# Optimization experiments

Measured on AMD Instinct MI355X. Metric: run time of the kernel, lower is better.

The kernel has to match this reference:

```python
import jax, jax.numpy as jnp
import numpy as np

T, B, I, H, LBL = 200, 1024, 128, 128, 4


def setup_inputs() -> dict:
    key = jax.random.key(0)
    ks = jax.random.split(key, 14)
    si = 1.0 / np.sqrt(I)
    sh = 1.0 / np.sqrt(H)
    inputs = jax.random.normal(ks[0], (T, B, I), jnp.float32)
    lengths = jnp.maximum(jax.random.randint(ks[1], (B,), 1, T + 1), LBL).astype(jnp.int32)
    return {
        "inputs": inputs,
        "lengths": lengths,
        "Wih_g": jax.random.normal(ks[2], (3 * H, I), jnp.float32) * si,
        "Whh_g": jax.random.normal(ks[3], (3 * H, H), jnp.float32) * sh,
        "bih_g": jax.random.normal(ks[4], (3 * H,), jnp.float32) * sh,
        "bhh_g": jax.random.normal(ks[5], (3 * H,), jnp.float32) * sh,
        "Wih_l": jax.random.normal(ks[6], (3 * H, I), jnp.float32) * si,
        "Whh_l": jax.random.normal(ks[7], (3 * H, H), jnp.float32) * sh,
        "bih_l": jax.random.normal(ks[8], (3 * H,), jnp.float32) * sh,
        "bhh_l": jax.random.normal(ks[9], (3 * H,), jnp.float32) * sh,
        "A1": jax.random.normal(ks[10], (H, H), jnp.float32) * sh,
        "A2": jax.random.normal(ks[11], (H, H), jnp.float32) * sh,
        "v1": jax.random.normal(ks[12], (1, H), jnp.float32) * sh,
        "label_len": LBL,
    }


def gru(x, Wih, Whh, bih, bhh):
    # x: [T, B, I] time-major. PyTorch GRU cell semantics.
    Bq, Hq = x.shape[1], Whh.shape[1]
    gi_all = jnp.einsum('tbi,gi->tbg', x, Wih) + bih  # precompute input projections [T,B,3H]
    def step(h, gi):
        gh = h @ Whh.T + bhh
        ir, iz, inn = jnp.split(gi, 3, axis=-1)
        hr, hz, hn = jnp.split(gh, 3, axis=-1)
        r = jax.nn.sigmoid(ir + hr)
        z = jax.nn.sigmoid(iz + hz)
        n = jnp.tanh(inn + r * hn)
        h = (1.0 - z) * n + z * h
        return h, h
    h0 = jnp.zeros((Bq, Hq), x.dtype)
    _, hs = jax.lax.scan(step, h0, gi_all)
    return hs  # [T, B, H]


def reference(inputs, lengths, Wih_g, Whh_g, bih_g, bhh_g,
              Wih_l, Whh_l, bih_l, bhh_l, A1, A2, v1, label_len):
    h_g = gru(inputs, Wih_g, Whh_g, bih_g, bhh_g)  # [T,B,H]
    h_l = gru(inputs, Wih_l, Whh_l, bih_l, bhh_l)  # [T,B,H]
    # attention score per step s: v1(sigmoid(A1 h_l + A2 h_g)), query-independent
    pre = jax.nn.sigmoid(jnp.einsum('tbh,gh->tbg', h_l, A1) +
                         jnp.einsum('tbh,gh->tbg', h_g, A2))
    scores = jnp.einsum('tbg,og->tbo', pre, v1)  # [T,B,1]
    # per-t output = cumsum_{s<=t}(score*h_l) + h_g[t]
    out = jnp.cumsum(scores * h_l, axis=0) + h_g  # [T,B,H]
    out_b = jnp.transpose(out, (1, 0, 2))  # [B,T,H]
    # gather last label_len timesteps of each sequence: h[b,k] = out[L_b-label_len+k, b]
    idx = lengths[:, None].astype(jnp.int32) - label_len + jnp.arange(label_len, dtype=jnp.int32)[None, :]
    idx = jnp.clip(idx, 0, out_b.shape[1] - 1)  # [B, label_len]
    h = jnp.take_along_axis(out_b, idx[:, :, None], axis=1)  # [B, label_len, H]
    return h
```

## Files before the change

kernel.cpp:

```cpp
#include <hip/hip_runtime.h>
#include <stdint.h>


typedef __attribute__((ext_vector_type(8))) short short8;
typedef __attribute__((ext_vector_type(4))) float float4v;

#define LDS_BARRIER() asm volatile("s_waitcnt lgkmcnt(0)\n\ts_barrier" ::: "memory")

__device__ inline float bf2f(unsigned short u){
  union { unsigned int i; float f; } v; v.i = ((unsigned int)u) << 16; return v.f;
}
__device__ inline unsigned short f2bf(float f){
  union { float f; unsigned int i; } v; v.f = f;
  unsigned int x = v.i;
  return (unsigned short)((x + 0x7fffu + ((x >> 16) & 1u)) >> 16);
}
__device__ inline unsigned int cvt_pk_bf16(float a, float b){
  unsigned int r;
  asm("v_cvt_pk_bf16_f32 %0, %1, %2" : "=v"(r) : "v"(a), "v"(b));
  return r;
}
__device__ inline float sigm(float x){ return __builtin_amdgcn_rcpf(1.0f + __expf(-x)); }

union __align__(16) LdsU {
  struct { unsigned short hbuf[2][16][136]; unsigned short xbuf[2][16][136]; } scan;
  struct {
    unsigned short hlL[25 * 544];
    unsigned short hgL[25 * 544];
    float part[8 * 112];
    float scR[112];
  } cm;
};

__global__ __launch_bounds__(512, 2) void k_fat(
    const float* __restrict__ x,
    const float* __restrict__ bih_g, const float* __restrict__ bhh_g,
    const float* __restrict__ bih_l, const float* __restrict__ bhh_l,
    const float* __restrict__ Wih_g, const float* __restrict__ Whh_g,
    const float* __restrict__ Wih_l, const float* __restrict__ Whh_l,
    unsigned short* __restrict__ wst, unsigned short* __restrict__ a12,
    const float* __restrict__ v1, const int* __restrict__ lengths,
    unsigned short* __restrict__ hl, unsigned short* __restrict__ hg,
    float* __restrict__ cum, float* __restrict__ out,
    int scan_t0, int sccum_t0, int sccum_base, int build)
{
  __shared__ LdsU lds;
  int tid = threadIdx.x;
  int bid = blockIdx.x;

  if (scan_t0 >= 0 && bid < 128) {
    const int tc = 100;
    int t0 = scan_t0;
    auto& hbuf = lds.scan.hbuf;
    auto& xbuf = lds.scan.xbuf;

    int w = tid >> 6, L = tid & 63, l15 = L & 15, q = L >> 4;
    int gru = bid & 1;
    int b0 = (bid >> 1) * 16;
    const float* bih = gru ? bih_l : bih_g;
    const float* bhh = gru ? bhh_l : bhh_g;
    unsigned short* myseq = gru ? hl : hg;

    int col = w * 16 + l15;

    short8 Wi[3][4], Wh[3][4];
    if (t0 == 0) {
      const float* Wih = gru ? Wih_l : Wih_g;
      const float* Whh = gru ? Whh_l : Whh_g;
      #pragma unroll
      for (int G = 0; G < 3; G++) {
        int row = G * 128 + col;
        #pragma unroll
        for (int kf = 0; kf < 4; kf++) {
          const float4* p0 = (const float4*)(Wih + (size_t)row * 128 + kf * 32 + q * 8);
          const float4* p1 = (const float4*)(Whh + (size_t)row * 128 + kf * 32 + q * 8);
          float4 a0 = p0[0], a1 = p0[1], b0f = p1[0], b1f = p1[1];
          short8 si, sh;
          si[0]=(short)f2bf(a0.x); si[1]=(short)f2bf(a0.y); si[2]=(short)f2bf(a0.z); si[3]=(short)f2bf(a0.w);
          si[4]=(short)f2bf(a1.x); si[5]=(short)f2bf(a1.y); si[6]=(short)f2bf(a1.z); si[7]=(short)f2bf(a1.w);
          sh[0]=(short)f2bf(b0f.x); sh[1]=(short)f2bf(b0f.y); sh[2]=(short)f2bf(b0f.z); sh[3]=(short)f2bf(b0f.w);
          sh[4]=(short)f2bf(b1f.x); sh[5]=(short)f2bf(b1f.y); sh[6]=(short)f2bf(b1f.z); sh[7]=(short)f2bf(b1f.w);
          Wi[G][kf] = si; Wh[G][kf] = sh;
        }
      }
    } else {
      int gmi = gru * 2;
      int gmh = gru * 2 + 1;
      #pragma unroll
      for (int G = 0; G < 3; G++) {
        #pragma unroll
        for (int kf = 0; kf < 4; kf++) {
          Wi[G][kf] = *(const short8*)(wst + (((size_t)((gmi * 3 + G) * 4 + kf)) << 12) + tid * 8);
          Wh[G][kf] = *(const short8*)(wst + (((size_t)((gmh * 3 + G) * 4 + kf)) << 12) + tid * 8);
        }
      }
    }
    float br  = bih[col]       + bhh[col];
    float bz  = bih[128 + col] + bhh[128 + col];
    float bin = bih[256 + col];
    float bnh = bhh[256 + col];

    float hold[4];
    if (t0 == 0) {
      #pragma unroll
      for (int r = 0; r < 4; r++) { hold[r] = 0.0f; hbuf[0][q * 4 + r][col] = 0; }
    } else {
      const unsigned short* carry = myseq + (size_t)(t0 - 1) * 131072;
      #pragma unroll
      for (int r = 0; r < 4; r++) {
        int m = q * 4 + r;
        unsigned short u = carry[(size_t)(b0 + m) * 128 + col];
        hold[r] = bf2f(u);
        hbuf[0][m][col] = u;
      }
    }
    int xrow = tid >> 5, xc4 = (tid & 31) * 4;
    size_t hoff = (size_t)b0 * 128 + xrow * 128 + xc4;
    {
      float4 x0 = ((const float4*)(x + ((size_t)t0 * 1024 + b0) * 128))[tid];
      *(uint2*)&xbuf[0][xrow][xc4] = make_uint2(cvt_pk_bf16(x0.x, x0.y), cvt_pk_bf16(x0.z, x0.w));
    }
    float4 xr = ((const float4*)(x + ((size_t)(t0 + 1) * 1024 + b0) * 128))[tid];
    __syncthreads();

    float4v cx0 = (float4v){0.f,0.f,0.f,0.f}, cx1 = cx0, cx2 = cx0;
    {
      short8 Ax[4];
      #pragma unroll
      for (int kf = 0; kf < 4; kf++) Ax[kf] = *(const short8*)&xbuf[0][l15][kf * 32 + q * 8];
      #pragma unroll
      for (int kf = 0; kf < 4; kf++) cx0 = __builtin_amdgcn_mfma_f32_16x16x32_bf16(Ax[kf], Wi[0][kf], cx0, 0,0,0);
      #pragma unroll
      for (int kf = 0; kf < 4; kf++) cx1 = __builtin_amdgcn_mfma_f32_16x16x32_bf16(Ax[kf], Wi[1][kf], cx1, 0,0,0);
      #pragma unroll
      for (int kf = 0; kf < 4; kf++) cx2 = __builtin_amdgcn_mfma_f32_16x16x32_bf16(Ax[kf], Wi[2][kf], cx2, 0,0,0);
    }
    *(uint2*)&xbuf[1][xrow][xc4] = make_uint2(cvt_pk_bf16(xr.x, xr.y), cvt_pk_bf16(xr.z, xr.w));
    xr = ((const float4*)(x + ((size_t)(t0 + 2) * 1024 + b0) * 128))[tid];
    LDS_BARRIER();

    auto step = [&](int s, int pin, int pout) {
      short8 Ah[4], Axn[4];
      #pragma unroll
      for (int kf = 0; kf < 4; kf++) Ah[kf]  = *(const short8*)&hbuf[pin][l15][kf * 32 + q * 8];
      #pragma unroll
      for (int kf = 0; kf < 4; kf++) Axn[kf] = *(const short8*)&xbuf[pout][l15][kf * 32 + q * 8];

      if (s > 0) {
        uint2 hv = *(const uint2*)&hbuf[pin][xrow][xc4];
        *(uint2*)(myseq + (size_t)(t0 + s - 1) * 131072 + hoff) = hv;
      }

      float4v rh = (float4v){0.f,0.f,0.f,0.f}, zh = rh, nh = rh;
      #pragma unroll
      for (int kf = 0; kf < 4; kf++) rh = __builtin_amdgcn_mfma_f32_16x16x32_bf16(Ah[kf], Wh[0][kf], rh, 0,0,0);
      #pragma unroll
      for (int kf = 0; kf < 4; kf++) zh = __builtin_amdgcn_mfma_f32_16x16x32_bf16(Ah[kf], Wh[1][kf], zh, 0,0,0);
      #pragma unroll
      for (int kf = 0; kf < 4; kf++) nh = __builtin_amdgcn_mfma_f32_16x16x32_bf16(Ah[kf], Wh[2][kf], nh, 0,0,0);

      float4v nx0 = (float4v){0.f,0.f,0.f,0.f}, nx1 = nx0, nx2 = nx0;
      #pragma unroll
      for (int kf = 0; kf < 4; kf++) nx0 = __builtin_amdgcn_mfma_f32_16x16x32_bf16(Axn[kf], Wi[0][kf], nx0, 0,0,0);
      #pragma unroll
      for (int kf = 0; kf < 4; kf++) nx1 = __builtin_amdgcn_mfma_f32_16x16x32_bf16(Axn[kf], Wi[1][kf], nx1, 0,0,0);
      #pragma unroll
      for (int kf = 0; kf < 4; kf++) nx2 = __builtin_amdgcn_mfma_f32_16x16x32_bf16(Axn[kf], Wi[2][kf], nx2, 0,0,0);

      *(uint2*)&xbuf[pin][xrow][xc4] = make_uint2(cvt_pk_bf16(xr.x, xr.y), cvt_pk_bf16(xr.z, xr.w));
      {
        int t3 = t0 + (s + 3 < tc ? s + 3 : tc - 1);
        xr = ((const float4*)(x + ((size_t)t3 * 1024 + b0) * 128))[tid];
      }

      float cr[4], cz[4], cn[4];
      #pragma unroll
      for (int r = 0; r < 4; r++) { cr[r] = cx0[r] + br; cz[r] = cx1[r] + bz; cn[r] = cx2[r] + bin; }

      float hnv[4];
      #pragma unroll
      for (int r = 0; r < 4; r++) {
        float er = __expf(-(rh[r] + cr[r]));
        float ez = __expf(-(zh[r] + cz[r]));
        float pr = 1.0f + er, pz = 1.0f + ez;
        float inv = __builtin_amdgcn_rcpf(pr * pz);
        float rr = pz * inv;
        float zz = pr * inv;
        float y  = cn[r] + rr * (nh[r] + bnh);
        float em = __expf(-2.0f * y);
        float nn = 2.0f * __builtin_amdgcn_rcpf(1.0f + em) - 1.0f;
        hnv[r] = nn + zz * (hold[r] - nn);
        hold[r] = hnv[r];
      }
      unsigned int p01 = cvt_pk_bf16(hnv[0], hnv[1]);
      unsigned int p23 = cvt_pk_bf16(hnv[2], hnv[3]);
      hbuf[pout][q * 4 + 0][col] = (unsigned short)p01;
      hbuf[pout][q * 4 + 1][col] = (unsigned short)(p01 >> 16);
      hbuf[pout][q * 4 + 2][col] = (unsigned short)p23;
      hbuf[pout][q * 4 + 3][col] = (unsigned short)(p23 >> 16);

      cx0 = nx0; cx1 = nx1; cx2 = nx2;
      LDS_BARRIER();
    };

    for (int s = 0; s + 1 < tc; s += 2) { step(s, 0, 1); step(s + 1, 1, 0); }
    {
      uint2 hv = *(const uint2*)&hbuf[tc & 1][xrow][xc4];
      *(uint2*)(myseq + (size_t)(t0 + tc - 1) * 131072 + hoff) = hv;
    }
    return;
  }

  if (build) {
    if (bid < 128) return;
    int gid = (bid - 128) * 512 + tid;
    (void)gid;
    return;
  }

  if (sccum_t0 >= 0) {
    int t0c = sccum_t0;
    int rb = bid - sccum_base;
    int b0c = rb * 4;
    int w = tid >> 6, L = tid & 63, l15 = L & 15, q = L >> 4;
    int jc = tid & 127, bc = tid >> 7;
    int b = b0c + bc;

    auto* hlL = lds.cm.hlL;
    auto* hgL = lds.cm.hgL;
    float* part = lds.cm.part;
    float* scR  = lds.cm.scR;

    float c = (t0c == 0) ? 0.0f : cum[(size_t)b * 128 + jc];
    int cap0 = lengths[b] - 4;

    float hgv[4];
    #pragma unroll
    for (int d = 0; d < 4; d++) {
      int sl = cap0 + d - t0c;
      hgv[d] = (sl >= 0 && sl < 100) ? bf2f(hg[((size_t)(cap0 + d) * 1024 + b) * 128 + jc]) : 0.f;
    }

    short8 B1[4], B2[4];
    #pragma unroll
    for (int kf = 0; kf < 4; kf++) {
      B1[kf] = *(const short8*)(a12 + (size_t)(w * 16 + l15) * 128 + kf * 32 + q * 8);
      B2[kf] = *(const short8*)(a12 + 16384 + (size_t)(w * 16 + l15) * 128 + kf * 32 + q * 8);
    }
    float v1w = v1[w * 16 + l15];

    for (int seg = 0; seg < 4; seg++) {
      int t0s = t0c + seg * 25;
      __syncthreads();
      for (int f8 = tid; f8 < 1600; f8 += 512) {
        int sl = f8 >> 6, r8 = f8 & 63, bb = r8 >> 4, j8 = r8 & 15;
        size_t gsrc = ((size_t)(t0s + sl) * 1024 + b0c) * 128 + r8 * 8;
        int dst = sl * 544 + bb * 136 + j8 * 8;
        *(short8*)&hlL[dst] = *(const short8*)(hl + gsrc);
        *(short8*)&hgL[dst] = *(const short8*)(hg + gsrc);
      }
      __syncthreads();

      #pragma unroll
      for (int T = 0; T < 7; T++) {
        int tl = T * 4 + (l15 >> 2); if (tl > 24) tl = 24;
        int bb = l15 & 3;
        int abase = tl * 544 + bb * 136 + q * 8;
        short8 Al[4], Ag[4];
        #pragma unroll
        for (int kf = 0; kf < 4; kf++) {
          Al[kf] = *(const short8*)&hlL[abase + kf * 32];
          Ag[kf] = *(const short8*)&hgL[abase + kf * 32];
        }
        float4v acc = (float4v){0.f, 0.f, 0.f, 0.f};
        #pragma unroll
        for (int kf = 0; kf < 4; kf++) acc = __builtin_amdgcn_mfma_f32_16x16x32_bf16(Al[kf], B1[kf], acc, 0,0,0);
        #pragma unroll
        for (int kf = 0; kf < 4; kf++) acc = __builtin_amdgcn_mfma_f32_16x16x32_bf16(Ag[kf], B2[kf], acc, 0,0,0);
        #pragma unroll
        for (int r = 0; r < 4; r++) {
          float sv = v1w * sigm(acc[r]);
          sv += __shfl_xor(sv, 1, 16);
          sv += __shfl_xor(sv, 2, 16);
          sv += __shfl_xor(sv, 4, 16);
          sv += __shfl_xor(sv, 8, 16);
          if (l15 == 0) part[w * 112 + T * 16 + q * 4 + r] = sv;
        }
      }
      __syncthreads();
      if (tid < 100) {
        float s = 0.f;
        #pragma unroll
        for (int w8 = 0; w8 < 8; w8++) s += part[w8 * 112 + tid];
        scR[tid] = s;
      }
      __syncthreads();

      for (int sl = 0; sl < 25; sl += 5) {
        float h[5], scv[5];
        #pragma unroll
        for (int k = 0; k < 5; k++) {
          h[k]  = bf2f(hlL[(sl + k) * 544 + bc * 136 + jc]);
          scv[k] = scR[(sl + k) * 4 + bc];
        }
        #pragma unroll
        for (int k = 0; k < 5; k++) {
          c += scv[k] * h[k];
          int d = (t0s + sl + k) - cap0;
          if ((unsigned)d < 4u)
            out[((size_t)b * 4 + d) * 128 + jc] = c + hgv[d];
        }
      }
    }
    cum[(size_t)b * 128 + jc] = c;
    return;
  }
}

__global__ __launch_bounds__(512) void k_build(
    const float* __restrict__ Wih_g, const float* __restrict__ Whh_g,
    const float* __restrict__ Wih_l, const float* __restrict__ Whh_l,
    const float* __restrict__ A1, const float* __restrict__ A2,
    unsigned short* __restrict__ wst, unsigned short* __restrict__ a12)
{
  int gid = blockIdx.x * 512 + threadIdx.x;
  if (gid < 32768) a12[gid] = f2bf((gid < 16384) ? A1[gid] : A2[gid - 16384]);
  #pragma unroll
  for (int k = 0; k < 3; k++) {
    int i = gid + k * 65536;
    int f = i >> 12;
    int r = i & 4095;
    int t = r >> 3, e = r & 7;
    int l15 = t & 15, q = (t >> 4) & 3, wv = t >> 6;
    int col = wv * 16 + l15;
    int kf = f & 3, g3 = f >> 2;
    int G = g3 % 3, gm = g3 / 3;
    const float* src = (gm == 0) ? Wih_g : (gm == 1) ? Whh_g : (gm == 2) ? Wih_l : Whh_l;
    int row = G * 128 + col;
    int kk = kf * 32 + q * 8 + e;
    wst[i] = f2bf(src[(size_t)row * 128 + kk]);
  }
}

extern "C" void kernel_launch(void* const* d_in, const int* in_sizes, int n_in,
                              void* d_out, int out_size, void* d_ws, size_t ws_size,
                              hipStream_t stream)
{
  const float* x     = (const float*)d_in[0];
  const int* lengths = (const int*)d_in[1];
  const float* Wih_g = (const float*)d_in[2];
  const float* Whh_g = (const float*)d_in[3];
  const float* bih_g = (const float*)d_in[4];
  const float* bhh_g = (const float*)d_in[5];
  const float* Wih_l = (const float*)d_in[6];
  const float* Whh_l = (const float*)d_in[7];
  const float* bih_l = (const float*)d_in[8];
  const float* bhh_l = (const float*)d_in[9];
  const float* A1    = (const float*)d_in[10];
  const float* A2    = (const float*)d_in[11];
  const float* v1    = (const float*)d_in[12];
  float* out = (float*)d_out;

  char* wsb = (char*)d_ws;
  size_t o = 0;
  unsigned short* a12 = (unsigned short*)(wsb + o); o += 65536;
  unsigned short* wst = (unsigned short*)(wsb + o); o += 393216;
  float* cum          = (float*)(wsb + o);          o += 524288;
  unsigned short* hl  = (unsigned short*)(wsb + o); o += (size_t)200 * 1024 * 128 * 2;
  unsigned short* hg  = (unsigned short*)(wsb + o); o += (size_t)200 * 1024 * 128 * 2;
  if (o > ws_size) return;

  k_build<<<128, 512, 0, stream>>>(Wih_g, Whh_g, Wih_l, Whh_l, A1, A2, wst, a12);
  k_fat<<<128, 512, 0, stream>>>(x, bih_g, bhh_g, bih_l, bhh_l,
                                 Wih_g, Whh_g, Wih_l, Whh_l,
                                 wst, a12, v1, lengths, hl, hg, cum, out,
                                 0, -1, 0, 0);
  k_fat<<<384, 512, 0, stream>>>(x, bih_g, bhh_g, bih_l, bhh_l,
                                 Wih_g, Whh_g, Wih_l, Whh_l,
                                 wst, a12, v1, lengths, hl, hg, cum, out,
                                 100, 0, 128, 0);
  k_fat<<<256, 512, 0, stream>>>(x, bih_g, bhh_g, bih_l, bhh_l,
                                 Wih_g, Whh_g, Wih_l, Whh_l,
                                 wst, a12, v1, lengths, hl, hg, cum, out,
                                 -1, 100, 0, 0);
}
```

Before: 398.6 us.

## Run full-length GRU scan with 4-row batch tiles, then a single score/cumsum pass

```diff
diff --git a/kernel.cpp b/kernel.cpp
--- a/kernel.cpp
+++ b/kernel.cpp
@@ -22,323 +22,260 @@
 }
 __device__ inline float sigm(float x){ return __builtin_amdgcn_rcpf(1.0f + __expf(-x)); }
 
-union __align__(16) LdsU {
-  struct { unsigned short hbuf[2][16][136]; unsigned short xbuf[2][16][136]; } scan;
-  struct {
-    unsigned short hlL[25 * 544];
-    unsigned short hgL[25 * 544];
-    float part[8 * 112];
-    float scR[112];
-  } cm;
-};
-
-__global__ __launch_bounds__(512, 2) void k_fat(
+__global__ __launch_bounds__(512, 2) void k_scan(
     const float* __restrict__ x,
+    const float* __restrict__ Wih_g, const float* __restrict__ Whh_g,
     const float* __restrict__ bih_g, const float* __restrict__ bhh_g,
+    const float* __restrict__ Wih_l, const float* __restrict__ Whh_l,
     const float* __restrict__ bih_l, const float* __restrict__ bhh_l,
-    const float* __restrict__ Wih_g, const float* __restrict__ Whh_g,
-    const float* __restrict__ Wih_l, const float* __restrict__ Whh_l,
-    unsigned short* __restrict__ wst, unsigned short* __restrict__ a12,
+    unsigned short* __restrict__ hl_seq, unsigned short* __restrict__ hg_seq)
+{
+  __shared__ __align__(16) unsigned short hbuf[2][16][136];
+  __shared__ __align__(16) unsigned short xbuf[2][16][136];
+  const int tc = 200;
+  int tid = threadIdx.x;
+  int w = tid >> 6, L = tid & 63, l15 = L & 15, q = L >> 4;
+  int gru = blockIdx.x & 1;
+  int b0 = (blockIdx.x >> 1) * 4;
+  const float* Wih = gru ? Wih_l : Wih_g;
+  const float* Whh = gru ? Whh_l : Whh_g;
+  const float* bih = gru ? bih_l : bih_g;
+  const float* bhh = gru ? bhh_l : bhh_g;
+  unsigned short* myseq = gru ? hl_seq : hg_seq;
+
+  int col = w * 16 + l15;
+
+  short8 Wi[3][4], Wh[3][4];
+  #pragma unroll
+  for (int G = 0; G < 3; G++) {
+    int row = G * 128 + col;
+    #pragma unroll
+    for (int kf = 0; kf < 4; kf++) {
+      const float4* p0 = (const float4*)(Wih + (size_t)row * 128 + kf * 32 + q * 8);
+      const float4* p1 = (const float4*)(Whh + (size_t)row * 128 + kf * 32 + q * 8);
+      float4 a0 = p0[0], a1 = p0[1], b0f = p1[0], b1f = p1[1];
+      short8 si, sh;
+      si[0]=(short)f2bf(a0.x); si[1]=(short)f2bf(a0.y); si[2]=(short)f2bf(a0.z); si[3]=(short)f2bf(a0.w);
+      si[4]=(short)f2bf(a1.x); si[5]=(short)f2bf(a1.y); si[6]=(short)f2bf(a1.z); si[7]=(short)f2bf(a1.w);
+      sh[0]=(short)f2bf(b0f.x); sh[1]=(short)f2bf(b0f.y); sh[2]=(short)f2bf(b0f.z); sh[3]=(short)f2bf(b0f.w);
+      sh[4]=(short)f2bf(b1f.x); sh[5]=(short)f2bf(b1f.y); sh[6]=(short)f2bf(b1f.z); sh[7]=(short)f2bf(b1f.w);
+      Wi[G][kf] = si; Wh[G][kf] = sh;
+    }
+  }
+  float br  = bih[col]       + bhh[col];
+  float bz  = bih[128 + col] + bhh[128 + col];
+  float bin = bih[256 + col];
+  float bnh = bhh[256 + col];
+
+  float hold[4] = {0.f, 0.f, 0.f, 0.f};
+  #pragma unroll
+  for (int r = 0; r < 4; r++) hbuf[0][q * 4 + r][col] = 0;
+
+  int xrow = tid >> 5, xc4 = (tid & 31) * 4;
+  if (xrow >= 4) {
+    *(uint2*)&xbuf[0][xrow][xc4] = make_uint2(0u, 0u);
+    *(uint2*)&xbuf[1][xrow][xc4] = make_uint2(0u, 0u);
+  }
+  size_t hoff = (size_t)(b0 + xrow) * 128 + xc4;
+  float4 xr = make_float4(0.f, 0.f, 0.f, 0.f);
+  if (tid < 128) {
+    float4 x0 = *(const float4*)(x + ((size_t)0 * 1024 + b0) * 128 + tid * 4);
+    *(uint2*)&xbuf[0][xrow][xc4] = make_uint2(cvt_pk_bf16(x0.x, x0.y), cvt_pk_bf16(x0.z, x0.w));
+    xr = *(const float4*)(x + ((size_t)1 * 1024 + b0) * 128 + tid * 4);
+  }
+  __syncthreads();
+
+  float4v cx0 = (float4v){0.f,0.f,0.f,0.f}, cx1 = cx0, cx2 = cx0;
+  {
+    short8 Ax[4];
+    #pragma unroll
+    for (int kf = 0; kf < 4; kf++) Ax[kf] = *(const short8*)&xbuf[0][l15][kf * 32 + q * 8];
+    #pragma unroll
+    for (int kf = 0; kf < 4; kf++) cx0 = __builtin_amdgcn_mfma_f32_16x16x32_bf16(Ax[kf], Wi[0][kf], cx0, 0,0,0);
+    #pragma unroll
+    for (int kf = 0; kf < 4; kf++) cx1 = __builtin_amdgcn_mfma_f32_16x16x32_bf16(Ax[kf], Wi[1][kf], cx1, 0,0,0);
+    #pragma unroll
+    for (int kf = 0; kf < 4; kf++) cx2 = __builtin_amdgcn_mfma_f32_16x16x32_bf16(Ax[kf], Wi[2][kf], cx2, 0,0,0);
+  }
+  if (tid < 128) {
+    *(uint2*)&xbuf[1][xrow][xc4] = make_uint2(cvt_pk_bf16(xr.x, xr.y), cvt_pk_bf16(xr.z, xr.w));
+    xr = *(const float4*)(x + ((size_t)2 * 1024 + b0) * 128 + tid * 4);
+  }
+  LDS_BARRIER();
+
+  auto step = [&](int s, int pin, int pout) {
+    short8 Ah[4], Axn[4];
+    #pragma unroll
+    for (int kf = 0; kf < 4; kf++) Ah[kf]  = *(const short8*)&hbuf[pin][l15][kf * 32 + q * 8];
+    #pragma unroll
+    for (int kf = 0; kf < 4; kf++) Axn[kf] = *(const short8*)&xbuf[pout][l15][kf * 32 + q * 8];
+
+    if (s > 0 && tid < 128) {
+      uint2 hv = *(const uint2*)&hbuf[pin][xrow][xc4];
+      *(uint2*)(myseq + (size_t)(s - 1) * 131072 + hoff) = hv;
+    }
+
+    float4v rh = (float4v){0.f,0.f,0.f,0.f}, zh = rh, nh = rh;
+    #pragma unroll
+    for (int kf = 0; kf < 4; kf++) rh = __builtin_amdgcn_mfma_f32_16x16x32_bf16(Ah[kf], Wh[0][kf], rh, 0,0,0);
+    #pragma unroll
+    for (int kf = 0; kf < 4; kf++) zh = __builtin_amdgcn_mfma_f32_16x16x32_bf16(Ah[kf], Wh[1][kf], zh, 0,0,0);
+    #pragma unroll
+    for (int kf = 0; kf < 4; kf++) nh = __builtin_amdgcn_mfma_f32_16x16x32_bf16(Ah[kf], Wh[2][kf], nh, 0,0,0);
+
+    float4v nx0 = (float4v){0.f,0.f,0.f,0.f}, nx1 = nx0, nx2 = nx0;
+    #pragma unroll
+    for (int kf = 0; kf < 4; kf++) nx0 = __builtin_amdgcn_mfma_f32_16x16x32_bf16(Axn[kf], Wi[0][kf], nx0, 0,0,0);
+    #pragma unroll
+    for (int kf = 0; kf < 4; kf++) nx1 = __builtin_amdgcn_mfma_f32_16x16x32_bf16(Axn[kf], Wi[1][kf], nx1, 0,0,0);
+    #pragma unroll
+    for (int kf = 0; kf < 4; kf++) nx2 = __builtin_amdgcn_mfma_f32_16x16x32_bf16(Axn[kf], Wi[2][kf], nx2, 0,0,0);
+
+    if (tid < 128) {
+      *(uint2*)&xbuf[pin][xrow][xc4] = make_uint2(cvt_pk_bf16(xr.x, xr.y), cvt_pk_bf16(xr.z, xr.w));
+      int t3 = (s + 3 < tc ? s + 3 : tc - 1);
+      xr = *(const float4*)(x + ((size_t)t3 * 1024 + b0) * 128 + tid * 4);
+    }
+
+    float cr[4], cz[4], cn[4];
+    #pragma unroll
+    for (int r = 0; r < 4; r++) { cr[r] = cx0[r] + br; cz[r] = cx1[r] + bz; cn[r] = cx2[r] + bin; }
+
+    float hnv[4];
+    #pragma unroll
+    for (int r = 0; r < 4; r++) {
+      float er = __expf(-(rh[r] + cr[r]));
+      float ez = __expf(-(zh[r] + cz[r]));
+      float pr = 1.0f + er, pz = 1.0f + ez;
+      float inv = __builtin_amdgcn_rcpf(pr * pz);
+      float rr = pz * inv;
+      float zz = pr * inv;
+      float y  = cn[r] + rr * (nh[r] + bnh);
+      float em = __expf(-2.0f * y);
+      float nn = 2.0f * __builtin_amdgcn_rcpf(1.0f + em) - 1.0f;
+      hnv[r] = nn + zz * (hold[r] - nn);
+      hold[r] = hnv[r];
+    }
+    unsigned int p01 = cvt_pk_bf16(hnv[0], hnv[1]);
+    unsigned int p23 = cvt_pk_bf16(hnv[2], hnv[3]);
+    hbuf[pout][q * 4 + 0][col] = (unsigned short)p01;
+    hbuf[pout][q * 4 + 1][col] = (unsigned short)(p01 >> 16);
+    hbuf[pout][q * 4 + 2][col] = (unsigned short)p23;
+    hbuf[pout][q * 4 + 3][col] = (unsigned short)(p23 >> 16);
+
+    cx0 = nx0; cx1 = nx1; cx2 = nx2;
+    LDS_BARRIER();
+  };
+
+  for (int s = 0; s + 1 < tc; s += 2) { step(s, 0, 1); step(s + 1, 1, 0); }
+  if (tid < 128) {
+    uint2 hv = *(const uint2*)&hbuf[tc & 1][xrow][xc4];
+    *(uint2*)(myseq + (size_t)(tc - 1) * 131072 + hoff) = hv;
+  }
+}
+
+__global__ __launch_bounds__(512, 2) void k_sccum(
+    const unsigned short* __restrict__ hl, const unsigned short* __restrict__ hg,
+    const float* __restrict__ A1, const float* __restrict__ A2,
     const float* __restrict__ v1, const int* __restrict__ lengths,
-    unsigned short* __restrict__ hl, unsigned short* __restrict__ hg,
-    float* __restrict__ cum, float* __restrict__ out,
-    int scan_t0, int sccum_t0, int sccum_base, int build)
+    float* __restrict__ out)
 {
-  __shared__ LdsU lds;
+  __shared__ __align__(16) unsigned short hlL[25 * 544];
+  __shared__ __align__(16) unsigned short hgL[25 * 544];
+  __shared__ float part[8 * 112];
+  __shared__ float scR[112];
   int tid = threadIdx.x;
-  int bid = blockIdx.x;
-
-  if (scan_t0 >= 0 && bid < 128) {
-    const int tc = 100;
-    int t0 = scan_t0;
-    auto& hbuf = lds.scan.hbuf;
-    auto& xbuf = lds.scan.xbuf;
-
-    int w = tid >> 6, L = tid & 63, l15 = L & 15, q = L >> 4;
-    int gru = bid & 1;
-    int b0 = (bid >> 1) * 16;
-    const float* bih = gru ? bih_l : bih_g;
-    const float* bhh = gru ? bhh_l : bhh_g;
-    unsigned short* myseq = gru ? hl : hg;
-
-    int col = w * 16 + l15;
-
-    short8 Wi[3][4], Wh[3][4];
-    if (t0 == 0) {
-      const float* Wih = gru ? Wih_l : Wih_g;
-      const float* Whh = gru ? Whh_l : Whh_g;
-      #pragma unroll
-      for (int G = 0; G < 3; G++) {
-        int row = G * 128 + col;
-        #pragma unroll
-        for (int kf = 0; kf < 4; kf++) {
-          const float4* p0 = (const float4*)(Wih + (size_t)row * 128 + kf * 32 + q * 8);
-          const float4* p1 = (const float4*)(Whh + (size_t)row * 128 + kf * 32 + q * 8);
-          float4 a0 = p0[0], a1 = p0[1], b0f = p1[0], b1f = p1[1];
-          short8 si, sh;
-          si[0]=(short)f2bf(a0.x); si[1]=(short)f2bf(a0.y); si[2]=(short)f2bf(a0.z); si[3]=(short)f2bf(a0.w);
-          si[4]=(short)f2bf(a1.x); si[5]=(short)f2bf(a1.y); si[6]=(short)f2bf(a1.z); si[7]=(short)f2bf(a1.w);
-          sh[0]=(short)f2bf(b0f.x); sh[1]=(short)f2bf(b0f.y); sh[2]=(short)f2bf(b0f.z); sh[3]=(short)f2bf(b0f.w);
-          sh[4]=(short)f2bf(b1f.x); sh[5]=(short)f2bf(b1f.y); sh[6]=(short)f2bf(b1f.z); sh[7]=(short)f2bf(b1f.w);
-          Wi[G][kf] = si; Wh[G][kf] = sh;
-        }
+  int rb = blockIdx.x;
+  int b0c = rb * 4;
+  int w = tid >> 6, L = tid & 63, l15 = L & 15, q = L >> 4;
+  int jc = tid & 127, bc = (tid >> 7) & 3;
+  int b = b0c + bc;
+
+  float c = 0.0f;
+  int cap0 = lengths[b] - 4;
+
+  float hgv[4];
+  #pragma unroll
+  for (int d = 0; d < 4; d++)
+    hgv[d] = bf2f(hg[((size_t)(cap0 + d) * 1024 + b) * 128 + jc]);
+
+  short8 B1[4], B2[4];
+  #pragma unroll
+  for (int kf = 0; kf < 4; kf++) {
+    const float4* p1 = (const float4*)(A1 + (size_t)(w * 16 + l15) * 128 + kf * 32 + q * 8);
+    const float4* p2 = (const float4*)(A2 + (size_t)(w * 16 + l15) * 128 + kf * 32 + q * 8);
+    float4 a0 = p1[0], a1 = p1[1], c0 = p2[0], c1 = p2[1];
+    short8 s1, s2;
+    s1[0]=(short)f2bf(a0.x); s1[1]=(short)f2bf(a0.y); s1[2]=(short)f2bf(a0.z); s1[3]=(short)f2bf(a0.w);
+    s1[4]=(short)f2bf(a1.x); s1[5]=(short)f2bf(a1.y); s1[6]=(short)f2bf(a1.z); s1[7]=(short)f2bf(a1.w);
+    s2[0]=(short)f2bf(c0.x); s2[1]=(short)f2bf(c0.y); s2[2]=(short)f2bf(c0.z); s2[3]=(short)f2bf(c0.w);
+    s2[4]=(short)f2bf(c1.x); s2[5]=(short)f2bf(c1.y); s2[6]=(short)f2bf(c1.z); s2[7]=(short)f2bf(c1.w);
+    B1[kf] = s1; B2[kf] = s2;
+  }
+  float v1w = v1[w * 16 + l15];
+
+  for (int seg = 0; seg < 8; seg++) {
+    int t0s = seg * 25;
+    __syncthreads();
+    for (int f8 = tid; f8 < 1600; f8 += 512) {
+      int sl = f8 >> 6, r8 = f8 & 63, bb = r8 >> 4, j8 = r8 & 15;
+      size_t gsrc = ((size_t)(t0s + sl) * 1024 + b0c) * 128 + r8 * 8;
+      int dst = sl * 544 + bb * 136 + j8 * 8;
+      *(short8*)&hlL[dst] = *(const short8*)(hl + gsrc);
+      *(short8*)&hgL[dst] = *(const short8*)(hg + gsrc);
+    }
+    __syncthreads();
+
+    #pragma unroll
+    for (int T = 0; T < 7; T++) {
+      int tl = T * 4 + (l15 >> 2); if (tl > 24) tl = 24;
+      int bb = l15 & 3;
+      int abase = tl * 544 + bb * 136 + q * 8;
+      short8 Al[4], Ag[4];
+      #pragma unroll
+      for (int kf = 0; kf < 4; kf++) {
+        Al[kf] = *(const short8*)&hlL[abase + kf * 32];
+        Ag[kf] = *(const short8*)&hgL[abase + kf * 32];
       }
-    } else {
-      int gmi = gru * 2;
-      int gmh = gru * 2 + 1;
-      #pragma unroll
-      for (int G = 0; G < 3; G++) {
-        #pragma unroll
-        for (int kf = 0; kf < 4; kf++) {
-          Wi[G][kf] = *(const short8*)(wst + (((size_t)((gmi * 3 + G) * 4 + kf)) << 12) + tid * 8);
-          Wh[G][kf] = *(const short8*)(wst + (((size_t)((gmh * 3 + G) * 4 + kf)) << 12) + tid * 8);
-        }
+      float4v acc = (float4v){0.f, 0.f, 0.f, 0.f};
+      #pragma unroll
+      for (int kf = 0; kf < 4; kf++) acc = __builtin_amdgcn_mfma_f32_16x16x32_bf16(Al[kf], B1[kf], acc, 0,0,0);
+      #pragma unroll
+      for (int kf = 0; kf < 4; kf++) acc = __builtin_amdgcn_mfma_f32_16x16x32_bf16(Ag[kf], B2[kf], acc, 0,0,0);
+      #pragma unroll
+      for (int r = 0; r < 4; r++) {
+        float sv = v1w * sigm(acc[r]);
+        sv += __shfl_xor(sv, 1, 16);
+        sv += __shfl_xor(sv, 2, 16);
+        sv += __shfl_xor(sv, 4, 16);
+        sv += __shfl_xor(sv, 8, 16);
+        if (l15 == 0) part[w * 112 + T * 16 + q * 4 + r] = sv;
       }
     }
-    float br  = bih[col]       + bhh[col];
-    float bz  = bih[128 + col] + bhh[128 + col];
-    float bin = bih[256 + col];
-    float bnh = bhh[256 + col];
-
-    float hold[4];
-    if (t0 == 0) {
-      #pragma unroll
-      for (int r = 0; r < 4; r++) { hold[r] = 0.0f; hbuf[0][q * 4 + r][col] = 0; }
-    } else {
-      const unsigned short* carry = myseq + (size_t)(t0 - 1) * 131072;
-      #pragma unroll
-      for (int r = 0; r < 4; r++) {
-        int m = q * 4 + r;
-        unsigned short u = carry[(size_t)(b0 + m) * 128 + col];
-        hold[r] = bf2f(u);
-        hbuf[0][m][col] = u;
+    __syncthreads();
+    if (tid < 100) {
+      float s = 0.f;
+      #pragma unroll
+      for (int w8 = 0; w8 < 8; w8++) s += part[w8 * 112 + tid];
+      scR[tid] = s;
+    }
+    __syncthreads();
+
+    for (int sl = 0; sl < 25; sl += 5) {
+      float h[5], scv[5];
+      #pragma unroll
+      for (int k = 0; k < 5; k++) {
+        h[k]   = bf2f(hlL[(sl + k) * 544 + bc * 136 + jc]);
+        scv[k] = scR[(sl + k) * 4 + bc];
       }
-    }
-    int xrow = tid >> 5, xc4 = (tid & 31) * 4;
-    size_t hoff = (size_t)b0 * 128 + xrow * 128 + xc4;
-    {
-      float4 x0 = ((const float4*)(x + ((size_t)t0 * 1024 + b0) * 128))[tid];
-      *(uint2*)&xbuf[0][xrow][xc4] = make_uint2(cvt_pk_bf16(x0.x, x0.y), cvt_pk_bf16(x0.z, x0.w));
-    }
-    float4 xr = ((const float4*)(x + ((size_t)(t0 + 1) * 1024 + b0) * 128))[tid];
-    __syncthreads();
-
-    float4v cx0 = (float4v){0.f,0.f,0.f,0.f}, cx1 = cx0, cx2 = cx0;
-    {
-      short8 Ax[4];
-      #pragma unroll
-      for (int kf = 0; kf < 4; kf++) Ax[kf] = *(const short8*)&xbuf[0][l15][kf * 32 + q * 8];
-      #pragma unroll
-      for (int kf = 0; kf < 4; kf++) cx0 = __builtin_amdgcn_mfma_f32_16x16x32_bf16(Ax[kf], Wi[0][kf], cx0, 0,0,0);
-      #pragma unroll
-      for (int kf = 0; kf < 4; kf++) cx1 = __builtin_amdgcn_mfma_f32_16x16x32_bf16(Ax[kf], Wi[1][kf], cx1, 0,0,0);
-      #pragma unroll
-      for (int kf = 0; kf < 4; kf++) cx2 = __builtin_amdgcn_mfma_f32_16x16x32_bf16(Ax[kf], Wi[2][kf], cx2, 0,0,0);
-    }
-    *(uint2*)&xbuf[1][xrow][xc4] = make_uint2(cvt_pk_bf16(xr.x, xr.y), cvt_pk_bf16(xr.z, xr.w));
-    xr = ((const float4*)(x + ((size_t)(t0 + 2) * 1024 + b0) * 128))[tid];
-    LDS_BARRIER();
-
-    auto step = [&](int s, int pin, int pout) {
-      short8 Ah[4], Axn[4];
-      #pragma unroll
-      for (int kf = 0; kf < 4; kf++) Ah[kf]  = *(const short8*)&hbuf[pin][l15][kf * 32 + q * 8];
-      #pragma unroll
-      for (int kf = 0; kf < 4; kf++) Axn[kf] = *(const short8*)&xbuf[pout][l15][kf * 32 + q * 8];
-
-      if (s > 0) {
-        uint2 hv = *(const uint2*)&hbuf[pin][xrow][xc4];
-        *(uint2*)(myseq + (size_t)(t0 + s - 1) * 131072 + hoff) = hv;
+      #pragma unroll
+      for (int k = 0; k < 5; k++) {
+        c += scv[k] * h[k];
+        int d = (t0s + sl + k) - cap0;
+        if ((unsigned)d < 4u)
+          out[((size_t)b * 4 + d) * 128 + jc] = c + hgv[d];
       }
-
-      float4v rh = (float4v){0.f,0.f,0.f,0.f}, zh = rh, nh = rh;
-      #pragma unroll
-      for (int kf = 0; kf < 4; kf++) rh = __builtin_amdgcn_mfma_f32_16x16x32_bf16(Ah[kf], Wh[0][kf], rh, 0,0,0);
-      #pragma unroll
-      for (int kf = 0; kf < 4; kf++) zh = __builtin_amdgcn_mfma_f32_16x16x32_bf16(Ah[kf], Wh[1][kf], zh, 0,0,0);
-      #pragma unroll
-      for (int kf = 0; kf < 4; kf++) nh = __builtin_amdgcn_mfma_f32_16x16x32_bf16(Ah[kf], Wh[2][kf], nh, 0,0,0);
-
-      float4v nx0 = (float4v){0.f,0.f,0.f,0.f}, nx1 = nx0, nx2 = nx0;
-      #pragma unroll
-      for (int kf = 0; kf < 4; kf++) nx0 = __builtin_amdgcn_mfma_f32_16x16x32_bf16(Axn[kf], Wi[0][kf], nx0, 0,0,0);
-      #pragma unroll
-      for (int kf = 0; kf < 4; kf++) nx1 = __builtin_amdgcn_mfma_f32_16x16x32_bf16(Axn[kf], Wi[1][kf], nx1, 0,0,0);
-      #pragma unroll
-      for (int kf = 0; kf < 4; kf++) nx2 = __builtin_amdgcn_mfma_f32_16x16x32_bf16(Axn[kf], Wi[2][kf], nx2, 0,0,0);
-
-      *(uint2*)&xbuf[pin][xrow][xc4] = make_uint2(cvt_pk_bf16(xr.x, xr.y), cvt_pk_bf16(xr.z, xr.w));
-      {
-        int t3 = t0 + (s + 3 < tc ? s + 3 : tc - 1);
-        xr = ((const float4*)(x + ((size_t)t3 * 1024 + b0) * 128))[tid];
-      }
-
-      float cr[4], cz[4], cn[4];
-      #pragma unroll
-      for (int r = 0; r < 4; r++) { cr[r] = cx0[r] + br; cz[r] = cx1[r] + bz; cn[r] = cx2[r] + bin; }
-
-      float hnv[4];
-      #pragma unroll
-      for (int r = 0; r < 4; r++) {
-        float er = __expf(-(rh[r] + cr[r]));
-        float ez = __expf(-(zh[r] + cz[r]));
-        float pr = 1.0f + er, pz = 1.0f + ez;
-        float inv = __builtin_amdgcn_rcpf(pr * pz);
-        float rr = pz * inv;
-        float zz = pr * inv;
-        float y  = cn[r] + rr * (nh[r] + bnh);
-        float em = __expf(-2.0f * y);
-        float nn = 2.0f * __builtin_amdgcn_rcpf(1.0f + em) - 1.0f;
-        hnv[r] = nn + zz * (hold[r] - nn);
-        hold[r] = hnv[r];
-      }
-      unsigned int p01 = cvt_pk_bf16(hnv[0], hnv[1]);
-      unsigned int p23 = cvt_pk_bf16(hnv[2], hnv[3]);
-      hbuf[pout][q * 4 + 0][col] = (unsigned short)p01;
-      hbuf[pout][q * 4 + 1][col] = (unsigned short)(p01 >> 16);
-      hbuf[pout][q * 4 + 2][col] = (unsigned short)p23;
-      hbuf[pout][q * 4 + 3][col] = (unsigned short)(p23 >> 16);
-
-      cx0 = nx0; cx1 = nx1; cx2 = nx2;
-      LDS_BARRIER();
-    };
-
-    for (int s = 0; s + 1 < tc; s += 2) { step(s, 0, 1); step(s + 1, 1, 0); }
-    {
-      uint2 hv = *(const uint2*)&hbuf[tc & 1][xrow][xc4];
-      *(uint2*)(myseq + (size_t)(t0 + tc - 1) * 131072 + hoff) = hv;
-    }
-    return;
-  }
-
-  if (build) {
-    if (bid < 128) return;
-    int gid = (bid - 128) * 512 + tid;
-    (void)gid;
-    return;
-  }
-
-  if (sccum_t0 >= 0) {
-    int t0c = sccum_t0;
-    int rb = bid - sccum_base;
-    int b0c = rb * 4;
-    int w = tid >> 6, L = tid & 63, l15 = L & 15, q = L >> 4;
-    int jc = tid & 127, bc = tid >> 7;
-    int b = b0c + bc;
-
-    auto* hlL = lds.cm.hlL;
-    auto* hgL = lds.cm.hgL;
-    float* part = lds.cm.part;
-    float* scR  = lds.cm.scR;
-
-    float c = (t0c == 0) ? 0.0f : cum[(size_t)b * 128 + jc];
-    int cap0 = lengths[b] - 4;
-
-    float hgv[4];
-    #pragma unroll
-    for (int d = 0; d < 4; d++) {
-      int sl = cap0 + d - t0c;
-      hgv[d] = (sl >= 0 && sl < 100) ? bf2f(hg[((size_t)(cap0 + d) * 1024 + b) * 128 + jc]) : 0.f;
-    }
-
-    short8 B1[4], B2[4];
-    #pragma unroll
-    for (int kf = 0; kf < 4; kf++) {
-      B1[kf] = *(const short8*)(a12 + (size_t)(w * 16 + l15) * 128 + kf * 32 + q * 8);
-      B2[kf] = *(const short8*)(a12 + 16384 + (size_t)(w * 16 + l15) * 128 + kf * 32 + q * 8);
-    }
-    float v1w = v1[w * 16 + l15];
-
-    for (int seg = 0; seg < 4; seg++) {
-      int t0s = t0c + seg * 25;
-      __syncthreads();
-      for (int f8 = tid; f8 < 1600; f8 += 512) {
-        int sl = f8 >> 6, r8 = f8 & 63, bb = r8 >> 4, j8 = r8 & 15;
-        size_t gsrc = ((size_t)(t0s + sl) * 1024 + b0c) * 128 + r8 * 8;
-        int dst = sl * 544 + bb * 136 + j8 * 8;
-        *(short8*)&hlL[dst] = *(const short8*)(hl + gsrc);
-        *(short8*)&hgL[dst] = *(const short8*)(hg + gsrc);
-      }
-      __syncthreads();
-
-      #pragma unroll
-      for (int T = 0; T < 7; T++) {
-        int tl = T * 4 + (l15 >> 2); if (tl > 24) tl = 24;
-        int bb = l15 & 3;
-        int abase = tl * 544 + bb * 136 + q * 8;
-        short8 Al[4], Ag[4];
-        #pragma unroll
-        for (int kf = 0; kf < 4; kf++) {
-          Al[kf] = *(const short8*)&hlL[abase + kf * 32];
-          Ag[kf] = *(const short8*)&hgL[abase + kf * 32];
-        }
-        float4v acc = (float4v){0.f, 0.f, 0.f, 0.f};
-        #pragma unroll
-        for (int kf = 0; kf < 4; kf++) acc = __builtin_amdgcn_mfma_f32_16x16x32_bf16(Al[kf], B1[kf], acc, 0,0,0);
-        #pragma unroll
-        for (int kf = 0; kf < 4; kf++) acc = __builtin_amdgcn_mfma_f32_16x16x32_bf16(Ag[kf], B2[kf], acc, 0,0,0);
-        #pragma unroll
-        for (int r = 0; r < 4; r++) {
-          float sv = v1w * sigm(acc[r]);
-          sv += __shfl_xor(sv, 1, 16);
-          sv += __shfl_xor(sv, 2, 16);
-          sv += __shfl_xor(sv, 4, 16);
-          sv += __shfl_xor(sv, 8, 16);
-          if (l15 == 0) part[w * 112 + T * 16 + q * 4 + r] = sv;
-        }
-      }
-      __syncthreads();
-      if (tid < 100) {
-        float s = 0.f;
-        #pragma unroll
-        for (int w8 = 0; w8 < 8; w8++) s += part[w8 * 112 + tid];
-        scR[tid] = s;
-      }
-      __syncthreads();
-
-      for (int sl = 0; sl < 25; sl += 5) {
-        float h[5], scv[5];
-        #pragma unroll
-        for (int k = 0; k < 5; k++) {
-          h[k]  = bf2f(hlL[(sl + k) * 544 + bc * 136 + jc]);
-          scv[k] = scR[(sl + k) * 4 + bc];
-        }
-        #pragma unroll
-        for (int k = 0; k < 5; k++) {
-          c += scv[k] * h[k];
-          int d = (t0s + sl + k) - cap0;
-          if ((unsigned)d < 4u)
-            out[((size_t)b * 4 + d) * 128 + jc] = c + hgv[d];
-        }
-      }
-    }
-    cum[(size_t)b * 128 + jc] = c;
-    return;
-  }
-}
-
-__global__ __launch_bounds__(512) void k_build(
-    const float* __restrict__ Wih_g, const float* __restrict__ Whh_g,
-    const float* __restrict__ Wih_l, const float* __restrict__ Whh_l,
-    const float* __restrict__ A1, const float* __restrict__ A2,
-    unsigned short* __restrict__ wst, unsigned short* __restrict__ a12)
-{
-  int gid = blockIdx.x * 512 + threadIdx.x;
-  if (gid < 32768) a12[gid] = f2bf((gid < 16384) ? A1[gid] : A2[gid - 16384]);
-  #pragma unroll
-  for (int k = 0; k < 3; k++) {
-    int i = gid + k * 65536;
-    int f = i >> 12;
-    int r = i & 4095;
-    int t = r >> 3, e = r & 7;
-    int l15 = t & 15, q = (t >> 4) & 3, wv = t >> 6;
-    int col = wv * 16 + l15;
-    int kf = f & 3, g3 = f >> 2;
-    int G = g3 % 3, gm = g3 / 3;
-    const float* src = (gm == 0) ? Wih_g : (gm == 1) ? Whh_g : (gm == 2) ? Wih_l : Whh_l;
-    int row = G * 128 + col;
-    int kk = kf * 32 + q * 8 + e;
-    wst[i] = f2bf(src[(size_t)row * 128 + kk]);
+    }
   }
 }
 
@@ -363,24 +300,11 @@
 
   char* wsb = (char*)d_ws;
   size_t o = 0;
-  unsigned short* a12 = (unsigned short*)(wsb + o); o += 65536;
-  unsigned short* wst = (unsigned short*)(wsb + o); o += 393216;
-  float* cum          = (float*)(wsb + o);          o += 524288;
-  unsigned short* hl  = (unsigned short*)(wsb + o); o += (size_t)200 * 1024 * 128 * 2;
-  unsigned short* hg  = (unsigned short*)(wsb + o); o += (size_t)200 * 1024 * 128 * 2;
+  unsigned short* hl = (unsigned short*)(wsb + o); o += (size_t)200 * 1024 * 128 * 2;
+  unsigned short* hg = (unsigned short*)(wsb + o); o += (size_t)200 * 1024 * 128 * 2;
   if (o > ws_size) return;
 
-  k_build<<<128, 512, 0, stream>>>(Wih_g, Whh_g, Wih_l, Whh_l, A1, A2, wst, a12);
-  k_fat<<<128, 512, 0, stream>>>(x, bih_g, bhh_g, bih_l, bhh_l,
-                                 Wih_g, Whh_g, Wih_l, Whh_l,
-                                 wst, a12, v1, lengths, hl, hg, cum, out,
-                                 0, -1, 0, 0);
-  k_fat<<<384, 512, 0, stream>>>(x, bih_g, bhh_g, bih_l, bhh_l,
-                                 Wih_g, Whh_g, Wih_l, Whh_l,
-                                 wst, a12, v1, lengths, hl, hg, cum, out,
-                                 100, 0, 128, 0);
-  k_fat<<<256, 512, 0, stream>>>(x, bih_g, bhh_g, bih_l, bhh_l,
-                                 Wih_g, Whh_g, Wih_l, Whh_l,
-                                 wst, a12, v1, lengths, hl, hg, cum, out,
-                                 -1, 100, 0, 0);
-}
+  k_scan<<<512, 512, 0, stream>>>(x, Wih_g, Whh_g, bih_g, bhh_g,
+                                  Wih_l, Whh_l, bih_l, bhh_l, hl, hg);
+  k_sccum<<<256, 512, 0, stream>>>(hl, hg, A1, A2, v1, lengths, out);
+}
```

Result: slower. 578.9 us (+45.2%).
